# Optimization experiments

Hardware: AMD Instinct MI355X
Metric: run time of the kernel (lower is better)

## Reference

```python
import jax, jax.numpy as jnp
import numpy as np

N_NODES = 50000
N_EDGES = 500000
IN_CH = 128
HID = 64
HEADS = 4
N_LAYERS = 3
OUT_CH = 16
N_GRAPHS = 64
NEG_SLOPE = 0.2  # PyG GATConv default


def setup_inputs() -> dict:
    key = jax.random.key(0)
    ks = jax.random.split(key, 20)
    inp = {
        'x': jax.random.normal(ks[0], (N_NODES, IN_CH), dtype=jnp.float32),
        'edge_attr': jax.random.normal(ks[1], (N_EDGES, 8), dtype=jnp.float32),
        'edge_index': jax.random.randint(ks[2], (2, N_EDGES), 0, N_NODES, dtype=jnp.int64),
        'batch': jnp.sort(jax.random.randint(ks[3], (N_NODES,), 0, N_GRAPHS, dtype=jnp.int64)),
    }
    kidx = 4
    in_dim = IN_CH
    for i in range(N_LAYERS):
        inp[f'W{i}'] = jax.random.normal(ks[kidx], (in_dim, HEADS * HID), dtype=jnp.float32) * (1.0 / np.sqrt(in_dim)); kidx += 1
        inp[f'asrc{i}'] = jax.random.normal(ks[kidx], (HEADS, HID), dtype=jnp.float32) * 0.1; kidx += 1
        inp[f'adst{i}'] = jax.random.normal(ks[kidx], (HEADS, HID), dtype=jnp.float32) * 0.1; kidx += 1
        inp[f'b{i}'] = jnp.zeros((HEADS * HID,), dtype=jnp.float32)
        in_dim = HEADS * HID
    inp['Wc'] = jax.random.normal(ks[kidx], (HEADS * HID, OUT_CH), dtype=jnp.float32) * (1.0 / np.sqrt(HEADS * HID)); kidx += 1
    inp['bc'] = jnp.zeros((OUT_CH,), dtype=jnp.float32)
    return inp


def _gat_layer(x, src, dst, W, asrc, adst, b):
    # x: [N, F_in] -> h: [N, H, C]
    N = x.shape[0]
    h = (x @ W).reshape(N, HEADS, HID)
    s_src = jnp.einsum('nhc,hc->nh', h, asrc)  # [N, H]
    s_dst = jnp.einsum('nhc,hc->nh', h, adst)
    e = jax.nn.leaky_relu(s_src[src] + s_dst[dst], NEG_SLOPE)  # [E, H]
    # segment softmax over incoming edges of each destination node
    m = jax.ops.segment_max(e, dst, num_segments=N)            # [N, H]
    ex = jnp.exp(e - m[dst])
    denom = jax.ops.segment_sum(ex, dst, num_segments=N)       # [N, H]
    alpha = ex / (denom[dst] + 1e-16)                           # [E, H]
    out = jax.ops.segment_sum(alpha[:, :, None] * h[src], dst, num_segments=N)  # [N, H, C]
    return out.reshape(N, HEADS * HID) + b


def reference(x, edge_attr, edge_index, batch,
              W0, asrc0, adst0, b0,
              W1, asrc1, adst1, b1,
              W2, asrc2, adst2, b2,
              Wc, bc):
    N = x.shape[0]
    loop = jnp.arange(N, dtype=edge_index.dtype)
    # PyG GATConv adds self-loops by default
    src = jnp.concatenate([edge_index[0], loop])
    dst = jnp.concatenate([edge_index[1], loop])
    params = [(W0, asrc0, adst0, b0), (W1, asrc1, adst1, b1), (W2, asrc2, adst2, b2)]
    h = x
    for (W, asrc, adst, b) in params:
        h = jax.nn.relu(_gat_layer(h, src, dst, W, asrc, adst, b))
        # nn.Dropout(0.5) is identity in eval mode
    pooled = jax.ops.segment_sum(h, batch, num_segments=N_GRAPHS)  # global_add_pool
    return pooled @ Wc + bc
```

## Files before the change

kernel.cpp:

```cpp
#include <hip/hip_runtime.h>
#include <hip/hip_bf16.h>

#define NNODES 50000
#define NEDGES 500000
#define INCH 128
#define HID 64
#define HEADS 4
#define FDIM 256
#define NGRAPHS 64
#define OUTCH 16
#define NEG_SLOPE 0.2f

#define BM 64
#define BN 256
#define BK 32

typedef float f32x4 __attribute__((ext_vector_type(4)));
typedef _Float16 f16x8 __attribute__((ext_vector_type(8)));
typedef _Float16 f16x4 __attribute__((ext_vector_type(4)));

__device__ inline void gld_lds16(const void* g, void* l) {
    __builtin_amdgcn_global_load_lds((__attribute__((address_space(1))) void*)g,
                                     (__attribute__((address_space(3))) void*)l, 16, 0, 0);
}


__global__ void k_hist(const int* __restrict__ dst, int E, int* __restrict__ counts) {
    int i = blockIdx.x * blockDim.x + threadIdx.x;
    if (i < E) atomicAdd(&counts[dst[i]], 1);
}

__global__ __launch_bounds__(256) void k_blocksum(const int* __restrict__ counts, int N,
                                                  int* __restrict__ bsum) {
    int idx = blockIdx.x * 256 + threadIdx.x;
    int v = (idx < N) ? counts[idx] : 0;
#pragma unroll
    for (int off = 32; off; off >>= 1) v += __shfl_xor(v, off);
    __shared__ int wsum[4];
    if ((threadIdx.x & 63) == 0) wsum[threadIdx.x >> 6] = v;
    __syncthreads();
    if (threadIdx.x == 0) bsum[blockIdx.x] = wsum[0] + wsum[1] + wsum[2] + wsum[3];
}

__global__ __launch_bounds__(256) void k_scanfinal(const int* __restrict__ counts,
                                                   const int* __restrict__ bsum, int N,
                                                   int* __restrict__ rowstart,
                                                   int* __restrict__ cursor) {
    __shared__ int tmp[256];
    __shared__ int wsum[4];
    int t = threadIdx.x, b = blockIdx.x;
    int p = 0;
    for (int i = t; i < b; i += 256) p += bsum[i];
#pragma unroll
    for (int off = 32; off; off >>= 1) p += __shfl_xor(p, off);
    int idx = b * 256 + t;
    int v = (idx < N) ? counts[idx] : 0;
    tmp[t] = v;
    if ((t & 63) == 0) wsum[t >> 6] = p;
    __syncthreads();
    int bp = wsum[0] + wsum[1] + wsum[2] + wsum[3];
    for (int off = 1; off < 256; off <<= 1) {
        int u = (t >= off) ? tmp[t - off] : 0;
        __syncthreads();
        tmp[t] += u;
        __syncthreads();
    }
    if (idx < N) {
        int incl = bp + tmp[t];
        rowstart[idx + 1] = incl;
        cursor[idx] = incl - v;
    }
    if (idx == 0) rowstart[0] = 0;
}

__global__ void k_scatter(const int* __restrict__ src, const int* __restrict__ dst, int E,
                          int* __restrict__ cursor, int* __restrict__ csr_src) {
    int i = blockIdx.x * blockDim.x + threadIdx.x;
    if (i < E) {
        int p = atomicAdd(&cursor[dst[i]], 1);
        csr_src[p] = src[i];
    }
}


__global__ void k_wdecomp(const float* __restrict__ W, _Float16* __restrict__ Wt, int K) {
    int i = blockIdx.x * 256 + threadIdx.x;
    if (i >= K * 256) return;
    int k = i >> 8, n = i & 255;
    Wt[n * K + k] = (_Float16)W[i];
}


__global__ void k_adecomp(const float* __restrict__ X, _Float16* __restrict__ Xf, int total4) {
    int i = blockIdx.x * 256 + threadIdx.x;
    if (i >= total4) return;
    float4 v = ((const float4*)X)[i];
    f16x4 o = {(_Float16)v.x, (_Float16)v.y, (_Float16)v.z, (_Float16)v.w};
    ((f16x4*)Xf)[i] = o;
}


__global__ __launch_bounds__(256) void k_gemm_mfma(
    const _Float16* __restrict__ A, const _Float16* __restrict__ B,
    const float* __restrict__ av, const float* __restrict__ dv,
    _Float16* __restrict__ Hf,
    float* __restrict__ ssrcO, float* __restrict__ sdstO, int M, int K) {
    __shared__ _Float16 sA[2][BM * BK];
    __shared__ _Float16 sB[2][BN * BK];

    const int t = threadIdx.x;
    const int row0 = blockIdx.x * BM;
    const int wv = t >> 6, ln = t & 63, lr = ln & 15, lk = ln >> 4;

    const int ar = wv * 16 + (ln >> 2);
    const int alc = (ln & 3) ^ ((ar >> 1) & 3);
    const size_t agoff = (size_t)min(row0 + ar, M - 1) * K + alc * 8;
    const int brr = wv * 16 + (ln >> 2);
    const int fsc = lk ^ ((lr >> 1) & 3);

    f32x4 acc[4][4] = {};
    const int nt = K / BK;

#define STAGE(tt, p)                                                        \
    do {                                                                    \
        int _k0 = (tt)*BK;                                                  \
        gld_lds16(A + agoff + _k0, &sA[p][wv * 512]);                       \
        _Pragma("unroll") for (int _j = 0; _j < 4; ++_j) {                  \
            int _br = _j * 64 + brr;                                        \
            int _blc = (ln & 3) ^ ((_br >> 1) & 3);                         \
            gld_lds16(B + (size_t)_br * K + _k0 + _blc * 8,                 \
                      &sB[p][_j * 2048 + wv * 512]);                        \
        }                                                                   \
    } while (0)

    STAGE(0, 0);
    __syncthreads();
    for (int tt = 0; tt < nt; ++tt) {
        int cur = tt & 1;
        if (tt + 1 < nt) STAGE(tt + 1, cur ^ 1);

        f16x8 af[4];
#pragma unroll
        for (int mi = 0; mi < 4; ++mi)
            af[mi] = *(const f16x8*)&sA[cur][(mi * 16 + lr) * BK + fsc * 8];
#pragma unroll
        for (int ni = 0; ni < 4; ++ni) {
            f16x8 bf = *(const f16x8*)&sB[cur][(wv * 64 + ni * 16 + lr) * BK + fsc * 8];
#pragma unroll
            for (int mi = 0; mi < 4; ++mi)
                acc[mi][ni] = __builtin_amdgcn_mfma_f32_16x16x32_f16(af[mi], bf, acc[mi][ni], 0, 0, 0);
        }
        __syncthreads();
    }
#undef STAGE

    float ps[4][4] = {}, pd[4][4] = {};
#pragma unroll
    for (int ni = 0; ni < 4; ++ni) {
        int col = wv * 64 + ni * 16 + lr;
        float a_s = av[col], a_d = dv[col];
#pragma unroll
        for (int mi = 0; mi < 4; ++mi) {
            f32x4 v = acc[mi][ni];
            int r = row0 + mi * 16 + lk * 4;
#pragma unroll
            for (int j = 0; j < 4; ++j) {
                if (r + j < M) Hf[(size_t)(r + j) * FDIM + col] = (_Float16)v[j];
                ps[mi][j] += v[j] * a_s;
                pd[mi][j] += v[j] * a_d;
            }
        }
    }
#pragma unroll
    for (int mi = 0; mi < 4; ++mi) {
#pragma unroll
        for (int j = 0; j < 4; ++j) {
            float s = ps[mi][j], q = pd[mi][j];
            s += __shfl_xor(s, 1); s += __shfl_xor(s, 2);
            s += __shfl_xor(s, 4); s += __shfl_xor(s, 8);
            q += __shfl_xor(q, 1); q += __shfl_xor(q, 2);
            q += __shfl_xor(q, 4); q += __shfl_xor(q, 8);
            if (lr == 0) {
                int r = row0 + mi * 16 + lk * 4 + j;
                if (r < M) {
                    ssrcO[r * HEADS + wv] = s;
                    sdstO[r * HEADS + wv] = q;
                }
            }
        }
    }
}


__global__ __launch_bounds__(256) void k_aggregate(
    const _Float16* __restrict__ hf,
    const float* __restrict__ ssrc, const float* __restrict__ sdst,
    const int* __restrict__ rowstart, const int* __restrict__ csr_src,
    const float* __restrict__ bias,
    _Float16* __restrict__ outf, int N) {
    int wv = threadIdx.x >> 6, ln = threadIdx.x & 63;
    int n = blockIdx.x * 4 + wv;
    if (n >= N) return;
    int head = ln >> 4;
    int fo = head * 64 + (ln & 15) * 4;
    float sd = sdst[n * HEADS + head];
    float e = ssrc[n * HEADS + head] + sd;
    e = (e > 0.f) ? e : NEG_SLOPE * e;
    float m = e, d = 1.0f;
    f16x4 sv = *(const f16x4*)&hf[(size_t)n * FDIM + fo];
    float4 acc = make_float4((float)sv[0], (float)sv[1], (float)sv[2], (float)sv[3]);
    int r0 = rowstart[n], r1 = rowstart[n + 1];
    int cnt = r1 - r0;
    for (int base = 0; base < cnt; base += 8) {
        int s[8];
        f16x4 u[8];
        float c[8], w[8];
#pragma unroll
        for (int i = 0; i < 8; ++i) s[i] = csr_src[min(r0 + base + i, r1 - 1)];
#pragma unroll
        for (int i = 0; i < 8; ++i) u[i] = *(const f16x4*)&hf[(size_t)s[i] * FDIM + fo];
#pragma unroll
        for (int i = 0; i < 8; ++i) {
            float sc = ssrc[s[i] * HEADS + head] + sd;
            sc = (sc > 0.f) ? sc : NEG_SLOPE * sc;
            c[i] = (base + i < cnt) ? sc : -1e30f;
        }
        float mx = fmaxf(fmaxf(fmaxf(c[0], c[1]), fmaxf(c[2], c[3])),
                         fmaxf(fmaxf(c[4], c[5]), fmaxf(c[6], c[7])));
        float mn = fmaxf(m, mx);
        float wa = __expf(m - mn);
#pragma unroll
        for (int i = 0; i < 8; ++i) w[i] = __expf(c[i] - mn);
        float sx = 0.f, sy = 0.f, sz = 0.f, sw = 0.f, sdn = 0.f;
#pragma unroll
        for (int i = 0; i < 8; ++i) {
            sx += w[i] * (float)u[i][0];
            sy += w[i] * (float)u[i][1];
            sz += w[i] * (float)u[i][2];
            sw += w[i] * (float)u[i][3];
            sdn += w[i];
        }
        acc.x = acc.x * wa + sx;
        acc.y = acc.y * wa + sy;
        acc.z = acc.z * wa + sz;
        acc.w = acc.w * wa + sw;
        d = d * wa + sdn;
        m = mn;
    }
    float inv = 1.0f / d;
    float4 bv = *(const float4*)&bias[fo];
    f16x4 o;
    o[0] = (_Float16)fmaxf(acc.x * inv + bv.x, 0.f);
    o[1] = (_Float16)fmaxf(acc.y * inv + bv.y, 0.f);
    o[2] = (_Float16)fmaxf(acc.z * inv + bv.z, 0.f);
    o[3] = (_Float16)fmaxf(acc.w * inv + bv.w, 0.f);
    *(f16x4*)&outf[(size_t)n * FDIM + fo] = o;
}


__global__ __launch_bounds__(256) void k_pool(const _Float16* __restrict__ hf,
                                              const int* __restrict__ batch,
                                              float* __restrict__ pooled, int N) {
    int f = threadIdx.x;
    int n0 = blockIdx.x * 128;
    if (n0 >= N) return;
    int n1 = min(n0 + 128, N);
    int g = batch[n0];
    float run = 0.f;
    for (int n = n0; n < n1; ++n) {
        int gn = batch[n];
        if (gn != g) {
            atomicAdd(&pooled[g * FDIM + f], run);
            run = 0.f;
            g = gn;
        }
        run += (float)hf[(size_t)n * FDIM + f];
    }
    atomicAdd(&pooled[g * FDIM + f], run);
}


__global__ __launch_bounds__(256) void k_final(const float* __restrict__ pooled,
                                               const float* __restrict__ Wc,
                                               const float* __restrict__ bc,
                                               float* __restrict__ out) {
    int tid = blockIdx.x * 256 + threadIdx.x;
    int g = tid >> 4, o = tid & 15;
    float s = bc[o];
    for (int k = 0; k < FDIM; ++k) s += pooled[g * FDIM + k] * Wc[k * OUTCH + o];
    out[g * OUTCH + o] = s;
}


extern "C" void kernel_launch(void* const* d_in, const int* in_sizes, int n_in,
                              void* d_out, int out_size, void* d_ws, size_t ws_size,
                              hipStream_t stream) {
    const float* x = (const float*)d_in[0];
    const int* edge_index = (const int*)d_in[2];
    const int* batch = (const int*)d_in[3];
    const float* W[3]    = {(const float*)d_in[4], (const float*)d_in[8],  (const float*)d_in[12]};
    const float* asrc[3] = {(const float*)d_in[5], (const float*)d_in[9],  (const float*)d_in[13]};
    const float* adst[3] = {(const float*)d_in[6], (const float*)d_in[10], (const float*)d_in[14]};
    const float* bias[3] = {(const float*)d_in[7], (const float*)d_in[11], (const float*)d_in[15]};
    const float* Wc = (const float*)d_in[16];
    const float* bc = (const float*)d_in[17];

    const int N = in_sizes[3];
    const int E = in_sizes[2] / 2;
    const int* e_src = edge_index;
    const int* e_dst = edge_index + E;

    char* ws = (char*)d_ws;
    size_t off = 0;
    _Float16* hb = (_Float16*)(ws + off); off += (size_t)N * FDIM * 2;
    _Float16* xf = (_Float16*)(ws + off); off += (size_t)N * INCH * 2;
    _Float16* P  = (_Float16*)(ws + off); off += (size_t)N * FDIM * 2;
    float* ssrc = (float*)(ws + off); off += (size_t)N * HEADS * 4;
    float* sdst = (float*)(ws + off); off += (size_t)N * HEADS * 4;
    int* rowstart = (int*)(ws + off); off += ((size_t)(N + 1) * 4 + 255) / 256 * 256;
    int* counts = (int*)(ws + off); off += (size_t)N * 4;
    int* cursor = (int*)(ws + off); off += (size_t)N * 4;
    int* csr_src = (int*)(ws + off); off += (size_t)E * 4;
    float* pooled = (float*)(ws + off); off += (size_t)NGRAPHS * FDIM * 4;
    int* bsum = (int*)(ws + off); off += ((size_t)((N + 255) / 256) * 4 + 255) / 256 * 256;
    _Float16* Wt[3];
    int Ks[3] = {INCH, FDIM, FDIM};
    for (int l = 0; l < 3; ++l) {
        Wt[l] = (_Float16*)(ws + off); off += (size_t)256 * Ks[l] * 2;
    }

    const int nb = (N + 255) / 256;

    hipMemsetAsync(counts, 0, (size_t)N * 4, stream);
    k_hist<<<(E + 255) / 256, 256, 0, stream>>>(e_dst, E, counts);
    k_blocksum<<<nb, 256, 0, stream>>>(counts, N, bsum);
    k_scanfinal<<<nb, 256, 0, stream>>>(counts, bsum, N, rowstart, cursor);
    k_scatter<<<(E + 255) / 256, 256, 0, stream>>>(e_src, e_dst, E, cursor, csr_src);

    k_adecomp<<<((N * INCH / 4) + 255) / 256, 256, 0, stream>>>(x, xf, N * INCH / 4);
    for (int l = 0; l < 3; ++l)
        k_wdecomp<<<(Ks[l] * 256 + 255) / 256, 256, 0, stream>>>(W[l], Wt[l], Ks[l]);

    const _Float16* Af = xf;
    for (int l = 0; l < 3; ++l) {
        int K = Ks[l];
        k_gemm_mfma<<<(N + BM - 1) / BM, 256, 0, stream>>>(Af, Wt[l], asrc[l], adst[l],
                                                           hb, ssrc, sdst, N, K);
        k_aggregate<<<(N + 3) / 4, 256, 0, stream>>>(hb, ssrc, sdst, rowstart, csr_src,
                                                     bias[l], P, N);
        Af = P;
    }

    hipMemsetAsync(pooled, 0, (size_t)NGRAPHS * FDIM * 4, stream);
    k_pool<<<(N + 127) / 128, 256, 0, stream>>>(P, batch, pooled, N);
    k_final<<<4, 256, 0, stream>>>(pooled, Wc, bc, (float*)d_out);
}
```

Measured before the change: 341.3 us.

## Precompute normalized edge softmax weights and enlarge GEMM row tile

Adds a k_edgew kernel that, for each (node, head), computes the segment-softmax max, denominator and normalized per-edge weights into a CSR-aligned buffer, plus the self-loop weight. The aggregation kernel then becomes a plain weighted sum with no online-softmax rescaling or exp work. The GEMM tile is doubled to 128 rows per block, with a launch-bounds occupancy hint and a restructured epilogue. The trade-off is an extra kernel per layer that walks each node's edge list three times with one thread per head, plus extra global traffic for the per-edge weights.

```diff
diff --git a/kernel.cpp b/kernel.cpp
--- a/kernel.cpp
+++ b/kernel.cpp
@@ -11,7 +11,7 @@
 #define OUTCH 16
 #define NEG_SLOPE 0.2f
 
-#define BM 64
+#define BM 128
 #define BN 256
 #define BK 32
 
@@ -100,7 +100,7 @@
 }
 
 
-__global__ __launch_bounds__(256) void k_gemm_mfma(
+__global__ __launch_bounds__(256, 2) void k_gemm_mfma(
     const _Float16* __restrict__ A, const _Float16* __restrict__ B,
     const float* __restrict__ av, const float* __restrict__ dv,
     _Float16* __restrict__ Hf,
@@ -114,21 +114,21 @@
 
     const int ar = wv * 16 + (ln >> 2);
     const int alc = (ln & 3) ^ ((ar >> 1) & 3);
-    const size_t agoff = (size_t)min(row0 + ar, M - 1) * K + alc * 8;
-    const int brr = wv * 16 + (ln >> 2);
+    const size_t agoff0 = (size_t)min(row0 + ar, M - 1) * K + alc * 8;
+    const size_t agoff1 = (size_t)min(row0 + ar + 64, M - 1) * K + alc * 8;
     const int fsc = lk ^ ((lr >> 1) & 3);
 
-    f32x4 acc[4][4] = {};
+    f32x4 acc[8][4] = {};
     const int nt = K / BK;
 
 #define STAGE(tt, p)                                                        \
     do {                                                                    \
         int _k0 = (tt)*BK;                                                  \
-        gld_lds16(A + agoff + _k0, &sA[p][wv * 512]);                       \
+        gld_lds16(A + agoff0 + _k0, &sA[p][wv * 512]);                      \
+        gld_lds16(A + agoff1 + _k0, &sA[p][2048 + wv * 512]);               \
         _Pragma("unroll") for (int _j = 0; _j < 4; ++_j) {                  \
-            int _br = _j * 64 + brr;                                        \
-            int _blc = (ln & 3) ^ ((_br >> 1) & 3);                         \
-            gld_lds16(B + (size_t)_br * K + _k0 + _blc * 8,                 \
+            int _br = _j * 64 + ar;                                         \
+            gld_lds16(B + (size_t)_br * K + _k0 + alc * 8,                  \
                       &sB[p][_j * 2048 + wv * 512]);                        \
         }                                                                   \
     } while (0)
@@ -139,62 +139,95 @@
         int cur = tt & 1;
         if (tt + 1 < nt) STAGE(tt + 1, cur ^ 1);
 
-        f16x8 af[4];
-#pragma unroll
-        for (int mi = 0; mi < 4; ++mi)
+        f16x8 af[8];
+#pragma unroll
+        for (int mi = 0; mi < 8; ++mi)
             af[mi] = *(const f16x8*)&sA[cur][(mi * 16 + lr) * BK + fsc * 8];
 #pragma unroll
         for (int ni = 0; ni < 4; ++ni) {
             f16x8 bf = *(const f16x8*)&sB[cur][(wv * 64 + ni * 16 + lr) * BK + fsc * 8];
 #pragma unroll
-            for (int mi = 0; mi < 4; ++mi)
+            for (int mi = 0; mi < 8; ++mi)
                 acc[mi][ni] = __builtin_amdgcn_mfma_f32_16x16x32_f16(af[mi], bf, acc[mi][ni], 0, 0, 0);
         }
         __syncthreads();
     }
 #undef STAGE
 
-    float ps[4][4] = {}, pd[4][4] = {};
+    float avr[4], dvr[4];
 #pragma unroll
     for (int ni = 0; ni < 4; ++ni) {
         int col = wv * 64 + ni * 16 + lr;
-        float a_s = av[col], a_d = dv[col];
-#pragma unroll
-        for (int mi = 0; mi < 4; ++mi) {
+        avr[ni] = av[col];
+        dvr[ni] = dv[col];
+    }
+#pragma unroll
+    for (int mi = 0; mi < 8; ++mi) {
+        float ps[4] = {}, pd[4] = {};
+        int rbase = row0 + mi * 16 + lk * 4;
+#pragma unroll
+        for (int ni = 0; ni < 4; ++ni) {
+            int col = wv * 64 + ni * 16 + lr;
             f32x4 v = acc[mi][ni];
-            int r = row0 + mi * 16 + lk * 4;
 #pragma unroll
             for (int j = 0; j < 4; ++j) {
-                if (r + j < M) Hf[(size_t)(r + j) * FDIM + col] = (_Float16)v[j];
-                ps[mi][j] += v[j] * a_s;
-                pd[mi][j] += v[j] * a_d;
+                if (rbase + j < M) Hf[(size_t)(rbase + j) * FDIM + col] = (_Float16)v[j];
+                ps[j] += v[j] * avr[ni];
+                pd[j] += v[j] * dvr[ni];
             }
         }
-    }
-#pragma unroll
-    for (int mi = 0; mi < 4; ++mi) {
 #pragma unroll
         for (int j = 0; j < 4; ++j) {
-            float s = ps[mi][j], q = pd[mi][j];
+            float s = ps[j], q = pd[j];
             s += __shfl_xor(s, 1); s += __shfl_xor(s, 2);
             s += __shfl_xor(s, 4); s += __shfl_xor(s, 8);
             q += __shfl_xor(q, 1); q += __shfl_xor(q, 2);
             q += __shfl_xor(q, 4); q += __shfl_xor(q, 8);
-            if (lr == 0) {
-                int r = row0 + mi * 16 + lk * 4 + j;
-                if (r < M) {
-                    ssrcO[r * HEADS + wv] = s;
-                    sdstO[r * HEADS + wv] = q;
-                }
+            if (lr == 0 && rbase + j < M) {
+                ssrcO[(rbase + j) * HEADS + wv] = s;
+                sdstO[(rbase + j) * HEADS + wv] = q;
             }
         }
     }
+}
+
+
+__global__ __launch_bounds__(256) void k_edgew(
+    const float* __restrict__ ssrc, const float* __restrict__ sdst,
+    const int* __restrict__ rowstart, const int* __restrict__ csr_src,
+    float* __restrict__ wcsr, float* __restrict__ aself, int N) {
+    int tid = blockIdx.x * 256 + threadIdx.x;
+    int n = tid >> 2, h = tid & 3;
+    if (n >= N) return;
+    int r0 = rowstart[n], r1 = rowstart[n + 1];
+    float sd = sdst[n * HEADS + h];
+    float es = ssrc[n * HEADS + h] + sd;
+    es = (es > 0.f) ? es : NEG_SLOPE * es;
+    float m = es;
+    for (int r = r0; r < r1; ++r) {
+        int s = csr_src[r];
+        float sc = ssrc[s * HEADS + h] + sd;
+        sc = (sc > 0.f) ? sc : NEG_SLOPE * sc;
+        m = fmaxf(m, sc);
+    }
+    float denom = __expf(es - m);
+    for (int r = r0; r < r1; ++r) {
+        int s = csr_src[r];
+        float sc = ssrc[s * HEADS + h] + sd;
+        sc = (sc > 0.f) ? sc : NEG_SLOPE * sc;
+        float w = __expf(sc - m);
+        wcsr[r * HEADS + h] = w;
+        denom += w;
+    }
+    float inv = 1.0f / denom;
+    aself[n * HEADS + h] = __expf(es - m) * inv;
+    for (int r = r0; r < r1; ++r) wcsr[r * HEADS + h] *= inv;
 }
 
 
 __global__ __launch_bounds__(256) void k_aggregate(
     const _Float16* __restrict__ hf,
-    const float* __restrict__ ssrc, const float* __restrict__ sdst,
+    const float* __restrict__ wcsr, const float* __restrict__ aself,
     const int* __restrict__ rowstart, const int* __restrict__ csr_src,
     const float* __restrict__ bias,
     _Float16* __restrict__ outf, int N) {
@@ -203,57 +236,40 @@
     if (n >= N) return;
     int head = ln >> 4;
     int fo = head * 64 + (ln & 15) * 4;
-    float sd = sdst[n * HEADS + head];
-    float e = ssrc[n * HEADS + head] + sd;
-    e = (e > 0.f) ? e : NEG_SLOPE * e;
-    float m = e, d = 1.0f;
+    float a0 = aself[n * HEADS + head];
     f16x4 sv = *(const f16x4*)&hf[(size_t)n * FDIM + fo];
-    float4 acc = make_float4((float)sv[0], (float)sv[1], (float)sv[2], (float)sv[3]);
+    float4 acc = make_float4(a0 * (float)sv[0], a0 * (float)sv[1],
+                             a0 * (float)sv[2], a0 * (float)sv[3]);
     int r0 = rowstart[n], r1 = rowstart[n + 1];
     int cnt = r1 - r0;
     for (int base = 0; base < cnt; base += 8) {
         int s[8];
+        float w[8];
         f16x4 u[8];
-        float c[8], w[8];
-#pragma unroll
-        for (int i = 0; i < 8; ++i) s[i] = csr_src[min(r0 + base + i, r1 - 1)];
+#pragma unroll
+        for (int i = 0; i < 8; ++i) {
+            int rr = min(r0 + base + i, r1 - 1);
+            s[i] = csr_src[rr];
+            w[i] = wcsr[rr * HEADS + head];
+        }
 #pragma unroll
         for (int i = 0; i < 8; ++i) u[i] = *(const f16x4*)&hf[(size_t)s[i] * FDIM + fo];
 #pragma unroll
+        for (int i = 0; i < 8; ++i) w[i] = (base + i < cnt) ? w[i] : 0.f;
+#pragma unroll
         for (int i = 0; i < 8; ++i) {
-            float sc = ssrc[s[i] * HEADS + head] + sd;
-            sc = (sc > 0.f) ? sc : NEG_SLOPE * sc;
-            c[i] = (base + i < cnt) ? sc : -1e30f;
-        }
-        float mx = fmaxf(fmaxf(fmaxf(c[0], c[1]), fmaxf(c[2], c[3])),
-                         fmaxf(fmaxf(c[4], c[5]), fmaxf(c[6], c[7])));
-        float mn = fmaxf(m, mx);
-        float wa = __expf(m - mn);
-#pragma unroll
-        for (int i = 0; i < 8; ++i) w[i] = __expf(c[i] - mn);
-        float sx = 0.f, sy = 0.f, sz = 0.f, sw = 0.f, sdn = 0.f;
-#pragma unroll
-        for (int i = 0; i < 8; ++i) {
-            sx += w[i] * (float)u[i][0];
-            sy += w[i] * (float)u[i][1];
-            sz += w[i] * (float)u[i][2];
-            sw += w[i] * (float)u[i][3];
-            sdn += w[i];
-        }
-        acc.x = acc.x * wa + sx;
-        acc.y = acc.y * wa + sy;
-        acc.z = acc.z * wa + sz;
-        acc.w = acc.w * wa + sw;
-        d = d * wa + sdn;
-        m = mn;
-    }
-    float inv = 1.0f / d;
+            acc.x += w[i] * (float)u[i][0];
+            acc.y += w[i] * (float)u[i][1];
+            acc.z += w[i] * (float)u[i][2];
+            acc.w += w[i] * (float)u[i][3];
+        }
+    }
     float4 bv = *(const float4*)&bias[fo];
     f16x4 o;
-    o[0] = (_Float16)fmaxf(acc.x * inv + bv.x, 0.f);
-    o[1] = (_Float16)fmaxf(acc.y * inv + bv.y, 0.f);
-    o[2] = (_Float16)fmaxf(acc.z * inv + bv.z, 0.f);
-    o[3] = (_Float16)fmaxf(acc.w * inv + bv.w, 0.f);
+    o[0] = (_Float16)fmaxf(acc.x + bv.x, 0.f);
+    o[1] = (_Float16)fmaxf(acc.y + bv.y, 0.f);
+    o[2] = (_Float16)fmaxf(acc.z + bv.z, 0.f);
+    o[3] = (_Float16)fmaxf(acc.w + bv.w, 0.f);
     *(f16x4*)&outf[(size_t)n * FDIM + fo] = o;
 }
 
@@ -317,6 +333,8 @@
     _Float16* P  = (_Float16*)(ws + off); off += (size_t)N * FDIM * 2;
     float* ssrc = (float*)(ws + off); off += (size_t)N * HEADS * 4;
     float* sdst = (float*)(ws + off); off += (size_t)N * HEADS * 4;
+    float* wcsr = (float*)(ws + off); off += (size_t)E * HEADS * 4;
+    float* aself = (float*)(ws + off); off += (size_t)N * HEADS * 4;
     int* rowstart = (int*)(ws + off); off += ((size_t)(N + 1) * 4 + 255) / 256 * 256;
     int* counts = (int*)(ws + off); off += (size_t)N * 4;
     int* cursor = (int*)(ws + off); off += (size_t)N * 4;
@@ -346,7 +364,9 @@
         int K = Ks[l];
         k_gemm_mfma<<<(N + BM - 1) / BM, 256, 0, stream>>>(Af, Wt[l], asrc[l], adst[l],
                                                            hb, ssrc, sdst, N, K);
-        k_aggregate<<<(N + 3) / 4, 256, 0, stream>>>(hb, ssrc, sdst, rowstart, csr_src,
+        k_edgew<<<(N * HEADS + 255) / 256, 256, 0, stream>>>(ssrc, sdst, rowstart, csr_src,
+                                                             wcsr, aself, N);
+        k_aggregate<<<(N + 3) / 4, 256, 0, stream>>>(hb, wcsr, aself, rowstart, csr_src,
                                                      bias[l], P, N);
         Af = P;
     }
```

New measurement: 386.4 us. +13.2%, slower.
